# Kernel tuning notes

Measured on AMD Instinct MI355X. Metric: run time of the kernel, lower is better.

Reference implementation:

```python
import jax, jax.numpy as jnp
import numpy as np

N_T = 2_000_000      # terrain nodes
E_SEQ = 2_000_000    # sequence edges
E_AS = 2_000_000     # assignment edges
N_TOR = 1_000_000    # torus nodes
E_TR = 8_000_000     # transport edges
TD, OD, PD, N_OPS = 4, 3, 1, 4  # terrain dim, torus dim, polarity dim, num operators


def setup_inputs() -> dict:
    key = jax.random.key(0)
    ks = jax.random.split(key, 12)
    inp = {
        "x_terrain": jax.random.normal(ks[0], (N_T, TD), jnp.float32),
        "polarity": jax.random.normal(ks[1], (E_AS, PD), jnp.float32),
        "x_torus": jax.random.normal(ks[2], (N_TOR, OD), jnp.float32),
        "seq_ei": jax.random.randint(ks[3], (2, E_SEQ), 0, N_T),
        "assign_src": jax.random.randint(ks[4], (E_AS,), 0, N_T),
        "assign_dst": jax.random.randint(ks[5], (E_AS,), 0, N_OPS),
        "tr_ei": jax.random.randint(ks[6], (2, E_TR), 0, N_TOR),
        # learned params (nn.Linear convention: y = x @ W.T + b)
        "W_seq": jax.random.normal(ks[7], (TD, TD), jnp.float32) * 0.5,      # SequenceConv.lin, no bias
        "op_W": jax.random.normal(ks[8], (N_OPS, TD, TD + PD), jnp.float32) * 0.4,
        "op_b": jax.random.normal(ks[9], (N_OPS, TD), jnp.float32) * 0.1,
        "gate_W": jax.random.normal(ks[10], (2 * OD, 1), jnp.float32) * 0.4,  # TransportConv.gate
        "gate_b": jax.random.normal(ks[11], (1,), jnp.float32) * 0.1,
    }
    return inp


def _engine_fwd(x_terrain, polarity, x_torus, W_seq, op_W, op_b, gate_W, gate_b,
                seq_ei, assign_src, assign_dst, tr_ei):
    # 1) SequenceConv: add-aggregated linear message along terrain cycle, residual add
    msg = x_terrain[seq_ei[0]] @ W_seq.T                       # [E_seq, TD]
    agg = jnp.zeros_like(x_terrain).at[seq_ei[1]].add(msg)     # scatter-add to dst
    x_t = x_terrain + agg

    # 2) per-node operator transform: first assignment edge per source node
    E = assign_src.shape[0]
    pos = jnp.arange(E, dtype=jnp.int32)
    first = jax.ops.segment_min(pos, assign_src, num_segments=x_t.shape[0])  # fill = int32 max
    has = first < E                                            # nodes with >=1 assignment
    fe = jnp.clip(first, 0, E - 1)
    op_idx = jnp.clip(assign_dst[fe], 0, op_W.shape[0] - 1)    # [N_T]
    pol = polarity[fe]                                         # [N_T, 1]
    inp = jnp.concatenate([x_t, pol], axis=-1)                 # [N_T, TD+1]
    out = jnp.einsum('nij,nj->ni', op_W[op_idx], inp) + op_b[op_idx]
    x_t = jnp.where(has[:, None], out, x_t)

    # 3) TransportConv: sigmoid-gated mean aggregation over torus edges, residual add
    src, dst = tr_ei[0], tr_ei[1]
    xi, xj = x_torus[dst], x_torus[src]
    gate = jax.nn.sigmoid(jnp.concatenate([xi, xj], axis=-1) @ gate_W + gate_b)  # [E_tr,1]
    m = gate * xj
    s = jax.ops.segment_sum(m, dst, num_segments=x_torus.shape[0])
    cnt = jax.ops.segment_sum(jnp.ones((m.shape[0],), m.dtype), dst,
                              num_segments=x_torus.shape[0])
    x_tor = x_torus + s / jnp.maximum(cnt, 1.0)[:, None]
    return x_t, x_tor


def reference(x_terrain, polarity, x_torus, seq_ei, assign_src, assign_dst, tr_ei,
              W_seq, op_W, op_b, gate_W, gate_b):
    return _engine_fwd(x_terrain, polarity, x_torus, W_seq, op_W, op_b, gate_W, gate_b,
                       seq_ei, assign_src, assign_dst, tr_ei)
```

## Files before the change

kernel.cpp:

```cpp
#include <hip/hip_runtime.h>
#include <hip/hip_fp16.h>
#include <math.h>

#define N_T   2000000
#define E_SEQ 2000000
#define E_AS  2000000
#define N_TOR 1000000
#define E_TR  8000000

typedef unsigned long long u64;

__device__ __forceinline__ long long center_field(u64 t, int bits) {
    long long h = 1LL << (bits - 1);
    return (long long)((t & ((1ULL << bits) - 1)) ^ (u64)h) - h;
}

__global__ __launch_bounds__(256) void seq_edge_kernel(
        const float4* __restrict__ x_terrain,
        const int* __restrict__ seq_src,
        const int* __restrict__ seq_dst,
        const float* __restrict__ W_seq,
        u64* __restrict__ agg_pk) {
    int e = blockIdx.x * blockDim.x + threadIdx.x;
    if (e >= E_SEQ) return;
    int s = seq_src[e];
    int d = seq_dst[e];
    float4 x = x_terrain[s];
    float m0 = fmaf(x.x, W_seq[0],  fmaf(x.y, W_seq[1],  fmaf(x.z, W_seq[2],  x.w * W_seq[3])));
    float m1 = fmaf(x.x, W_seq[4],  fmaf(x.y, W_seq[5],  fmaf(x.z, W_seq[6],  x.w * W_seq[7])));
    float m2 = fmaf(x.x, W_seq[8],  fmaf(x.y, W_seq[9],  fmaf(x.z, W_seq[10], x.w * W_seq[11])));
    float m3 = fmaf(x.x, W_seq[12], fmaf(x.y, W_seq[13], fmaf(x.z, W_seq[14], x.w * W_seq[15])));
    long long f0 = __float2int_rn(m0 * 256.0f);
    long long f1 = __float2int_rn(m1 * 256.0f);
    long long f2 = __float2int_rn(m2 * 256.0f);
    long long f3 = __float2int_rn(m3 * 256.0f);
    long long pk = f0 + (f1 << 16) + (f2 << 32) + (f3 << 48);
    atomicAdd(&agg_pk[d], (u64)pk);
}

__global__ __launch_bounds__(256) void assign_min_kernel(
        const int* __restrict__ assign_src,
        const int* __restrict__ assign_dst,
        const float* __restrict__ polarity,
        u64* __restrict__ first_pk) {
    int e = blockIdx.x * blockDim.x + threadIdx.x;
    if (e >= E_AS) return;
    int op = assign_dst[e] & 3;
    __half h = __float2half(polarity[e]);
    unsigned short hb;
    __builtin_memcpy(&hb, &h, 2);
    u64 key = ((u64)e << 18) | ((u64)op << 16) | (u64)hb;
    atomicMin(&first_pk[assign_src[e]], key);
}

__global__ __launch_bounds__(256) void terrain_node_kernel(
        const float4* __restrict__ x_terrain,
        const u64* __restrict__ agg_pk,
        const u64* __restrict__ first_pk,
        const float* __restrict__ op_W,
        const float* __restrict__ op_b,
        float4* __restrict__ out_xt) {
    int n = blockIdx.x * blockDim.x + threadIdx.x;
    if (n >= N_T) return;
    float4 x = x_terrain[n];
    u64 t = agg_pk[n];
    long long m0 = center_field(t, 16); t = (t - (u64)m0) >> 16;
    long long m1 = center_field(t, 16); t = (t - (u64)m1) >> 16;
    long long m2 = center_field(t, 16); t = (t - (u64)m2) >> 16;
    long long m3 = center_field(t, 16);
    const float inv = 1.0f / 256.0f;
    x.x += (float)m0 * inv; x.y += (float)m1 * inv;
    x.z += (float)m2 * inv; x.w += (float)m3 * inv;
    u64 fp = first_pk[n];
    if ((fp >> 18) < (u64)E_AS) {
        int op = (int)((fp >> 16) & 3);
        unsigned short hb = (unsigned short)(fp & 0xFFFF);
        __half h;
        __builtin_memcpy(&h, &hb, 2);
        float pol = __half2float(h);
        const float* W = op_W + op * 20;
        const float* b = op_b + op * 4;
        float4 o;
        o.x = fmaf(x.x, W[0],  fmaf(x.y, W[1],  fmaf(x.z, W[2],  fmaf(x.w, W[3],  fmaf(pol, W[4],  b[0])))));
        o.y = fmaf(x.x, W[5],  fmaf(x.y, W[6],  fmaf(x.z, W[7],  fmaf(x.w, W[8],  fmaf(pol, W[9],  b[1])))));
        o.z = fmaf(x.x, W[10], fmaf(x.y, W[11], fmaf(x.z, W[12], fmaf(x.w, W[13], fmaf(pol, W[14], b[2])))));
        o.w = fmaf(x.x, W[15], fmaf(x.y, W[16], fmaf(x.z, W[17], fmaf(x.w, W[18], fmaf(pol, W[19], b[3])))));
        x = o;
    }
    out_xt[n] = x;
}

__global__ __launch_bounds__(256) void torus_pre_kernel(
        const float* __restrict__ x_torus,
        const float* __restrict__ gate_W,
        const float* __restrict__ gate_b,
        float4* __restrict__ rec,
        float* __restrict__ zi_arr) {
    int n = blockIdx.x * blockDim.x + threadIdx.x;
    if (n >= N_TOR) return;
    const float* x = x_torus + (size_t)n * 3;
    float x0 = x[0], x1 = x[1], x2 = x[2];
    float zi = fmaf(x0, gate_W[0], fmaf(x1, gate_W[1], x2 * gate_W[2]));
    float zj = fmaf(x0, gate_W[3], fmaf(x1, gate_W[4],
               fmaf(x2, gate_W[5], gate_b[0])));
    rec[n] = make_float4(x0, x1, x2, zj);
    zi_arr[n] = zi;
}

__global__ __launch_bounds__(256) void tr_edge_kernel(
        const float4* __restrict__ rec,
        const float* __restrict__ zi_arr,
        const int* __restrict__ tr_src,
        const int* __restrict__ tr_dst,
        u64* __restrict__ tor_pk) {
    int e = blockIdx.x * blockDim.x + threadIdx.x;
    if (e >= E_TR) return;
    int si = tr_src[e];
    int di = tr_dst[e];
    float4 r = rec[si];
    float z = zi_arr[di] + r.w;
    float g = 1.0f / (1.0f + __expf(-z));
    long long f0 = __float2int_rn(g * r.x * 128.0f);
    long long f1 = __float2int_rn(g * r.y * 128.0f);
    long long f2 = __float2int_rn(g * r.z * 128.0f);
    long long pk = f0 + (f1 << 17) + (f2 << 34) + (1LL << 51);
    atomicAdd(&tor_pk[di], (u64)pk);
}

__global__ __launch_bounds__(256) void torus_node_kernel(
        const float* __restrict__ x_torus,
        const u64* __restrict__ tor_pk,
        float* __restrict__ out_tor) {
    int n = blockIdx.x * blockDim.x + threadIdx.x;
    if (n >= N_TOR) return;
    u64 t = tor_pk[n];
    long long m0 = center_field(t, 17); t = (t - (u64)m0) >> 17;
    long long m1 = center_field(t, 17); t = (t - (u64)m1) >> 17;
    long long m2 = center_field(t, 17); t = (t - (u64)m2) >> 17;
    float cnt = (float)(t & 0x1FFF);
    float inv = (1.0f / 128.0f) / fmaxf(cnt, 1.0f);
    size_t b = (size_t)n * 3;
    out_tor[b + 0] = x_torus[b + 0] + (float)m0 * inv;
    out_tor[b + 1] = x_torus[b + 1] + (float)m1 * inv;
    out_tor[b + 2] = x_torus[b + 2] + (float)m2 * inv;
}

extern "C" void kernel_launch(void* const* d_in, const int* in_sizes, int n_in,
                              void* d_out, int out_size, void* d_ws, size_t ws_size,
                              hipStream_t stream) {
    const float* x_terrain  = (const float*)d_in[0];
    const float* polarity   = (const float*)d_in[1];
    const float* x_torus    = (const float*)d_in[2];
    const int*   seq_ei     = (const int*)  d_in[3];
    const int*   assign_src = (const int*)  d_in[4];
    const int*   assign_dst = (const int*)  d_in[5];
    const int*   tr_ei      = (const int*)  d_in[6];
    const float* W_seq      = (const float*)d_in[7];
    const float* op_W       = (const float*)d_in[8];
    const float* op_b       = (const float*)d_in[9];
    const float* gate_W     = (const float*)d_in[10];
    const float* gate_b     = (const float*)d_in[11];

    float* out_xt  = (float*)d_out;
    float* out_tor = (float*)d_out + (size_t)N_T * 4;

    char* ws = (char*)d_ws;
    u64*    agg_pk   = (u64*)ws;
    u64*    first_pk = agg_pk + N_T;
    u64*    tor_pk   = first_pk + N_T;
    float4* rec      = (float4*)(tor_pk + N_TOR);
    float*  zi_arr   = (float*)(rec + N_TOR);

    hipMemsetAsync(agg_pk, 0, (size_t)N_T * 8, stream);
    hipMemsetAsync(first_pk, 0xFF, (size_t)N_T * 8, stream);
    hipMemsetAsync(tor_pk, 0, (size_t)N_TOR * 8, stream);

    const int B = 256;
    torus_pre_kernel<<<(N_TOR + B - 1) / B, B, 0, stream>>>(
        x_torus, gate_W, gate_b, rec, zi_arr);
    tr_edge_kernel<<<(E_TR + B - 1) / B, B, 0, stream>>>(
        rec, zi_arr, tr_ei, tr_ei + E_TR, tor_pk);
    seq_edge_kernel<<<(E_SEQ + B - 1) / B, B, 0, stream>>>(
        (const float4*)x_terrain, seq_ei, seq_ei + E_SEQ, W_seq, agg_pk);
    assign_min_kernel<<<(E_AS + B - 1) / B, B, 0, stream>>>(
        assign_src, assign_dst, polarity, first_pk);
    terrain_node_kernel<<<(N_T + B - 1) / B, B, 0, stream>>>(
        (const float4*)x_terrain, agg_pk, first_pk, op_W, op_b, (float4*)out_xt);
    torus_node_kernel<<<(N_TOR + B - 1) / B, B, 0, stream>>>(
        x_torus, tor_pk, out_tor);
}
```

Measured before the change: 719.9 us.

## Merge edge kernels and node kernels into two launches, drop torus precompute

Combines the three edge-phase kernels (transport, sequence, assignment) into one launch indexed by range, and the two node finalize kernels into another. Drops the torus precompute pass, so each transport edge now gathers both endpoints' 3-float features and computes the full gate dot product inline. This cuts kernel launches and the rec/zi workspace write and read, and lets the independent scatter phases overlap. In exchange each transport edge makes unaligned 3-float gathers of both endpoints instead of one float4 plus one float, and the fused kernels may branch divergently at range boundaries.

```diff
diff --git a/kernel.cpp b/kernel.cpp
--- a/kernel.cpp
+++ b/kernel.cpp
@@ -15,134 +15,120 @@
     return (long long)((t & ((1ULL << bits) - 1)) ^ (u64)h) - h;
 }
 
-__global__ __launch_bounds__(256) void seq_edge_kernel(
+__global__ __launch_bounds__(256) void edge_kernel(
+        const float* __restrict__ x_torus,
+        const int* __restrict__ tr_src,
+        const int* __restrict__ tr_dst,
+        const float* __restrict__ gate_W,
+        const float* __restrict__ gate_b,
+        u64* __restrict__ tor_pk,
         const float4* __restrict__ x_terrain,
         const int* __restrict__ seq_src,
         const int* __restrict__ seq_dst,
         const float* __restrict__ W_seq,
-        u64* __restrict__ agg_pk) {
-    int e = blockIdx.x * blockDim.x + threadIdx.x;
-    if (e >= E_SEQ) return;
-    int s = seq_src[e];
-    int d = seq_dst[e];
-    float4 x = x_terrain[s];
-    float m0 = fmaf(x.x, W_seq[0],  fmaf(x.y, W_seq[1],  fmaf(x.z, W_seq[2],  x.w * W_seq[3])));
-    float m1 = fmaf(x.x, W_seq[4],  fmaf(x.y, W_seq[5],  fmaf(x.z, W_seq[6],  x.w * W_seq[7])));
-    float m2 = fmaf(x.x, W_seq[8],  fmaf(x.y, W_seq[9],  fmaf(x.z, W_seq[10], x.w * W_seq[11])));
-    float m3 = fmaf(x.x, W_seq[12], fmaf(x.y, W_seq[13], fmaf(x.z, W_seq[14], x.w * W_seq[15])));
-    long long f0 = __float2int_rn(m0 * 256.0f);
-    long long f1 = __float2int_rn(m1 * 256.0f);
-    long long f2 = __float2int_rn(m2 * 256.0f);
-    long long f3 = __float2int_rn(m3 * 256.0f);
-    long long pk = f0 + (f1 << 16) + (f2 << 32) + (f3 << 48);
-    atomicAdd(&agg_pk[d], (u64)pk);
-}
-
-__global__ __launch_bounds__(256) void assign_min_kernel(
+        u64* __restrict__ agg_pk,
         const int* __restrict__ assign_src,
         const int* __restrict__ assign_dst,
         const float* __restrict__ polarity,
         u64* __restrict__ first_pk) {
-    int e = blockIdx.x * blockDim.x + threadIdx.x;
-    if (e >= E_AS) return;
-    int op = assign_dst[e] & 3;
-    __half h = __float2half(polarity[e]);
-    unsigned short hb;
-    __builtin_memcpy(&hb, &h, 2);
-    u64 key = ((u64)e << 18) | ((u64)op << 16) | (u64)hb;
-    atomicMin(&first_pk[assign_src[e]], key);
+    int i = blockIdx.x * blockDim.x + threadIdx.x;
+    if (i < E_TR) {
+        int e = i;
+        int si = tr_src[e];
+        int di = tr_dst[e];
+        const float* xi = x_torus + (size_t)di * 3;
+        const float* xj = x_torus + (size_t)si * 3;
+        float xj0 = xj[0], xj1 = xj[1], xj2 = xj[2];
+        float z = fmaf(xi[0], gate_W[0],
+                  fmaf(xi[1], gate_W[1],
+                  fmaf(xi[2], gate_W[2],
+                  fmaf(xj0,  gate_W[3],
+                  fmaf(xj1,  gate_W[4],
+                  fmaf(xj2,  gate_W[5], gate_b[0]))))));
+        float g = 1.0f / (1.0f + __expf(-z));
+        long long f0 = __float2int_rn(g * xj0 * 128.0f);
+        long long f1 = __float2int_rn(g * xj1 * 128.0f);
+        long long f2 = __float2int_rn(g * xj2 * 128.0f);
+        long long pk = f0 + (f1 << 17) + (f2 << 34) + (1LL << 51);
+        atomicAdd(&tor_pk[di], (u64)pk);
+    } else if (i < E_TR + E_SEQ) {
+        int e = i - E_TR;
+        int s = seq_src[e];
+        int d = seq_dst[e];
+        float4 x = x_terrain[s];
+        float m0 = fmaf(x.x, W_seq[0],  fmaf(x.y, W_seq[1],  fmaf(x.z, W_seq[2],  x.w * W_seq[3])));
+        float m1 = fmaf(x.x, W_seq[4],  fmaf(x.y, W_seq[5],  fmaf(x.z, W_seq[6],  x.w * W_seq[7])));
+        float m2 = fmaf(x.x, W_seq[8],  fmaf(x.y, W_seq[9],  fmaf(x.z, W_seq[10], x.w * W_seq[11])));
+        float m3 = fmaf(x.x, W_seq[12], fmaf(x.y, W_seq[13], fmaf(x.z, W_seq[14], x.w * W_seq[15])));
+        long long f0 = __float2int_rn(m0 * 256.0f);
+        long long f1 = __float2int_rn(m1 * 256.0f);
+        long long f2 = __float2int_rn(m2 * 256.0f);
+        long long f3 = __float2int_rn(m3 * 256.0f);
+        long long pk = f0 + (f1 << 16) + (f2 << 32) + (f3 << 48);
+        atomicAdd(&agg_pk[d], (u64)pk);
+    } else if (i < E_TR + E_SEQ + E_AS) {
+        int e = i - (E_TR + E_SEQ);
+        int op = assign_dst[e] & 3;
+        __half h = __float2half(polarity[e]);
+        unsigned short hb;
+        __builtin_memcpy(&hb, &h, 2);
+        u64 key = ((u64)e << 18) | ((u64)op << 16) | (u64)hb;
+        atomicMin(&first_pk[assign_src[e]], key);
+    }
 }
 
-__global__ __launch_bounds__(256) void terrain_node_kernel(
+__global__ __launch_bounds__(256) void node_kernel(
         const float4* __restrict__ x_terrain,
         const u64* __restrict__ agg_pk,
         const u64* __restrict__ first_pk,
         const float* __restrict__ op_W,
         const float* __restrict__ op_b,
-        float4* __restrict__ out_xt) {
-    int n = blockIdx.x * blockDim.x + threadIdx.x;
-    if (n >= N_T) return;
-    float4 x = x_terrain[n];
-    u64 t = agg_pk[n];
-    long long m0 = center_field(t, 16); t = (t - (u64)m0) >> 16;
-    long long m1 = center_field(t, 16); t = (t - (u64)m1) >> 16;
-    long long m2 = center_field(t, 16); t = (t - (u64)m2) >> 16;
-    long long m3 = center_field(t, 16);
-    const float inv = 1.0f / 256.0f;
-    x.x += (float)m0 * inv; x.y += (float)m1 * inv;
-    x.z += (float)m2 * inv; x.w += (float)m3 * inv;
-    u64 fp = first_pk[n];
-    if ((fp >> 18) < (u64)E_AS) {
-        int op = (int)((fp >> 16) & 3);
-        unsigned short hb = (unsigned short)(fp & 0xFFFF);
-        __half h;
-        __builtin_memcpy(&h, &hb, 2);
-        float pol = __half2float(h);
-        const float* W = op_W + op * 20;
-        const float* b = op_b + op * 4;
-        float4 o;
-        o.x = fmaf(x.x, W[0],  fmaf(x.y, W[1],  fmaf(x.z, W[2],  fmaf(x.w, W[3],  fmaf(pol, W[4],  b[0])))));
-        o.y = fmaf(x.x, W[5],  fmaf(x.y, W[6],  fmaf(x.z, W[7],  fmaf(x.w, W[8],  fmaf(pol, W[9],  b[1])))));
-        o.z = fmaf(x.x, W[10], fmaf(x.y, W[11], fmaf(x.z, W[12], fmaf(x.w, W[13], fmaf(pol, W[14], b[2])))));
-        o.w = fmaf(x.x, W[15], fmaf(x.y, W[16], fmaf(x.z, W[17], fmaf(x.w, W[18], fmaf(pol, W[19], b[3])))));
-        x = o;
-    }
-    out_xt[n] = x;
-}
-
-__global__ __launch_bounds__(256) void torus_pre_kernel(
-        const float* __restrict__ x_torus,
-        const float* __restrict__ gate_W,
-        const float* __restrict__ gate_b,
-        float4* __restrict__ rec,
-        float* __restrict__ zi_arr) {
-    int n = blockIdx.x * blockDim.x + threadIdx.x;
-    if (n >= N_TOR) return;
-    const float* x = x_torus + (size_t)n * 3;
-    float x0 = x[0], x1 = x[1], x2 = x[2];
-    float zi = fmaf(x0, gate_W[0], fmaf(x1, gate_W[1], x2 * gate_W[2]));
-    float zj = fmaf(x0, gate_W[3], fmaf(x1, gate_W[4],
-               fmaf(x2, gate_W[5], gate_b[0])));
-    rec[n] = make_float4(x0, x1, x2, zj);
-    zi_arr[n] = zi;
-}
-
-__global__ __launch_bounds__(256) void tr_edge_kernel(
-        const float4* __restrict__ rec,
-        const float* __restrict__ zi_arr,
-        const int* __restrict__ tr_src,
-        const int* __restrict__ tr_dst,
-        u64* __restrict__ tor_pk) {
-    int e = blockIdx.x * blockDim.x + threadIdx.x;
-    if (e >= E_TR) return;
-    int si = tr_src[e];
-    int di = tr_dst[e];
-    float4 r = rec[si];
-    float z = zi_arr[di] + r.w;
-    float g = 1.0f / (1.0f + __expf(-z));
-    long long f0 = __float2int_rn(g * r.x * 128.0f);
-    long long f1 = __float2int_rn(g * r.y * 128.0f);
-    long long f2 = __float2int_rn(g * r.z * 128.0f);
-    long long pk = f0 + (f1 << 17) + (f2 << 34) + (1LL << 51);
-    atomicAdd(&tor_pk[di], (u64)pk);
-}
-
-__global__ __launch_bounds__(256) void torus_node_kernel(
+        float4* __restrict__ out_xt,
         const float* __restrict__ x_torus,
         const u64* __restrict__ tor_pk,
         float* __restrict__ out_tor) {
-    int n = blockIdx.x * blockDim.x + threadIdx.x;
-    if (n >= N_TOR) return;
-    u64 t = tor_pk[n];
-    long long m0 = center_field(t, 17); t = (t - (u64)m0) >> 17;
-    long long m1 = center_field(t, 17); t = (t - (u64)m1) >> 17;
-    long long m2 = center_field(t, 17); t = (t - (u64)m2) >> 17;
-    float cnt = (float)(t & 0x1FFF);
-    float inv = (1.0f / 128.0f) / fmaxf(cnt, 1.0f);
-    size_t b = (size_t)n * 3;
-    out_tor[b + 0] = x_torus[b + 0] + (float)m0 * inv;
-    out_tor[b + 1] = x_torus[b + 1] + (float)m1 * inv;
-    out_tor[b + 2] = x_torus[b + 2] + (float)m2 * inv;
+    int i = blockIdx.x * blockDim.x + threadIdx.x;
+    if (i < N_T) {
+        int n = i;
+        float4 x = x_terrain[n];
+        u64 t = agg_pk[n];
+        long long m0 = center_field(t, 16); t = (t - (u64)m0) >> 16;
+        long long m1 = center_field(t, 16); t = (t - (u64)m1) >> 16;
+        long long m2 = center_field(t, 16); t = (t - (u64)m2) >> 16;
+        long long m3 = center_field(t, 16);
+        const float inv = 1.0f / 256.0f;
+        x.x += (float)m0 * inv; x.y += (float)m1 * inv;
+        x.z += (float)m2 * inv; x.w += (float)m3 * inv;
+        u64 fp = first_pk[n];
+        if ((fp >> 18) < (u64)E_AS) {
+            int op = (int)((fp >> 16) & 3);
+            unsigned short hb = (unsigned short)(fp & 0xFFFF);
+            __half h;
+            __builtin_memcpy(&h, &hb, 2);
+            float pol = __half2float(h);
+            const float* W = op_W + op * 20;
+            const float* b = op_b + op * 4;
+            float4 o;
+            o.x = fmaf(x.x, W[0],  fmaf(x.y, W[1],  fmaf(x.z, W[2],  fmaf(x.w, W[3],  fmaf(pol, W[4],  b[0])))));
+            o.y = fmaf(x.x, W[5],  fmaf(x.y, W[6],  fmaf(x.z, W[7],  fmaf(x.w, W[8],  fmaf(pol, W[9],  b[1])))));
+            o.z = fmaf(x.x, W[10], fmaf(x.y, W[11], fmaf(x.z, W[12], fmaf(x.w, W[13], fmaf(pol, W[14], b[2])))));
+            o.w = fmaf(x.x, W[15], fmaf(x.y, W[16], fmaf(x.z, W[17], fmaf(x.w, W[18], fmaf(pol, W[19], b[3])))));
+            x = o;
+        }
+        out_xt[n] = x;
+    } else if (i < N_T + N_TOR) {
+        int n = i - N_T;
+        u64 t = tor_pk[n];
+        long long m0 = center_field(t, 17); t = (t - (u64)m0) >> 17;
+        long long m1 = center_field(t, 17); t = (t - (u64)m1) >> 17;
+        long long m2 = center_field(t, 17); t = (t - (u64)m2) >> 17;
+        float cnt = (float)(t & 0x1FFF);
+        float inv = (1.0f / 128.0f) / fmaxf(cnt, 1.0f);
+        size_t b = (size_t)n * 3;
+        out_tor[b + 0] = x_torus[b + 0] + (float)m0 * inv;
+        out_tor[b + 1] = x_torus[b + 1] + (float)m1 * inv;
+        out_tor[b + 2] = x_torus[b + 2] + (float)m2 * inv;
+    }
 }
 
 extern "C" void kernel_launch(void* const* d_in, const int* in_sizes, int n_in,
@@ -165,27 +151,22 @@
     float* out_tor = (float*)d_out + (size_t)N_T * 4;
 
     char* ws = (char*)d_ws;
-    u64*    agg_pk   = (u64*)ws;
-    u64*    first_pk = agg_pk + N_T;
-    u64*    tor_pk   = first_pk + N_T;
-    float4* rec      = (float4*)(tor_pk + N_TOR);
-    float*  zi_arr   = (float*)(rec + N_TOR);
+    u64* agg_pk   = (u64*)ws;
+    u64* first_pk = agg_pk + N_T;
+    u64* tor_pk   = first_pk + N_T;
 
     hipMemsetAsync(agg_pk, 0, (size_t)N_T * 8, stream);
     hipMemsetAsync(first_pk, 0xFF, (size_t)N_T * 8, stream);
     hipMemsetAsync(tor_pk, 0, (size_t)N_TOR * 8, stream);
 
     const int B = 256;
-    torus_pre_kernel<<<(N_TOR + B - 1) / B, B, 0, stream>>>(
-        x_torus, gate_W, gate_b, rec, zi_arr);
-    tr_edge_kernel<<<(E_TR + B - 1) / B, B, 0, stream>>>(
-        rec, zi_arr, tr_ei, tr_ei + E_TR, tor_pk);
-    seq_edge_kernel<<<(E_SEQ + B - 1) / B, B, 0, stream>>>(
-        (const float4*)x_terrain, seq_ei, seq_ei + E_SEQ, W_seq, agg_pk);
-    assign_min_kernel<<<(E_AS + B - 1) / B, B, 0, stream>>>(
+    const long long total_e = (long long)E_TR + E_SEQ + E_AS;
+    edge_kernel<<<(int)((total_e + B - 1) / B), B, 0, stream>>>(
+        x_torus, tr_ei, tr_ei + E_TR, gate_W, gate_b, tor_pk,
+        (const float4*)x_terrain, seq_ei, seq_ei + E_SEQ, W_seq, agg_pk,
         assign_src, assign_dst, polarity, first_pk);
-    terrain_node_kernel<<<(N_T + B - 1) / B, B, 0, stream>>>(
-        (const float4*)x_terrain, agg_pk, first_pk, op_W, op_b, (float4*)out_xt);
-    torus_node_kernel<<<(N_TOR + B - 1) / B, B, 0, stream>>>(
+    const long long total_n = (long long)N_T + N_TOR;
+    node_kernel<<<(int)((total_n + B - 1) / B), B, 0, stream>>>(
+        (const float4*)x_terrain, agg_pk, first_pk, op_W, op_b, (float4*)out_xt,
         x_torus, tor_pk, out_tor);
 }
```

After: 692.6 us. 3.8% less time.
